# Performance work log

Measured on AMD Instinct MI355X. Metric: run time of the kernel, lower is better.

The kernel has to match this reference:

```python
import jax, jax.numpy as jnp
import numpy as np

NEG_SLOPE = 0.2

def gat_conv(x, W, a_src, a_dst, bias, src, dst, num_nodes, concat):
    # x: [N, F_in]; W: [F_in, H*C]; a_src/a_dst: [H, C]; src/dst: [E] (self-loops included)
    H, C = a_src.shape
    h = (x @ W).reshape(-1, H, C)                      # [N, H, C]
    alpha_s = jnp.einsum('nhc,hc->nh', h, a_src)       # [N, H]
    alpha_d = jnp.einsum('nhc,hc->nh', h, a_dst)       # [N, H]
    e = jax.nn.leaky_relu(alpha_s[src] + alpha_d[dst], NEG_SLOPE)  # [E, H]
    # segment softmax over destination nodes
    m = jax.ops.segment_max(e, dst, num_segments=num_nodes)        # [N, H]
    ex = jnp.exp(e - m[dst])
    denom = jax.ops.segment_sum(ex, dst, num_segments=num_nodes)   # [N, H]
    alpha = ex / (denom[dst] + 1e-16)                  # [E, H]
    msg = alpha[:, :, None] * h[src]                   # [E, H, C]
    out = jax.ops.segment_sum(msg, dst, num_segments=num_nodes)    # [N, H, C]
    if concat:
        out = out.reshape(num_nodes, H * C)
    else:
        out = out.mean(axis=1)
    return out + bias

def setup_inputs() -> dict:
    key = jax.random.key(0)
    ks = jax.random.split(key, 12)
    N, F_in, E = 100000, 512, 3200000
    H1, C1 = 8, 8
    OUT = 40
    x = jax.random.normal(ks[0], (N, F_in), dtype=jnp.float32)
    edge_index = jax.random.randint(ks[1], (2, E), 0, N, dtype=jnp.int64)
    glorot = lambda k, shape: jax.random.uniform(k, shape, jnp.float32, -1.0, 1.0) * np.sqrt(6.0 / (shape[0] + shape[-1]))
    W1 = glorot(ks[2], (F_in, H1 * C1))
    a_src1 = glorot(ks[3], (H1, C1))
    a_dst1 = glorot(ks[4], (H1, C1))
    b1 = jnp.zeros((H1 * C1,), jnp.float32)
    W2 = glorot(ks[5], (H1 * C1, OUT))
    a_src2 = glorot(ks[6], (1, OUT))
    a_dst2 = glorot(ks[7], (1, OUT))
    b2 = jnp.zeros((OUT,), jnp.float32)
    return {"x": x, "edge_index": edge_index, "W1": W1, "a_src1": a_src1,
            "a_dst1": a_dst1, "b1": b1, "W2": W2, "a_src2": a_src2,
            "a_dst2": a_dst2, "b2": b2}

def reference(x, edge_index, W1, a_src1, a_dst1, b1, W2, a_src2, a_dst2, b2):
    N = x.shape[0]
    loop = jnp.arange(N, dtype=edge_index.dtype)
    src = jnp.concatenate([edge_index[0], loop])  # add_self_loops=True (PyG default)
    dst = jnp.concatenate([edge_index[1], loop])
    # dropout is identity in eval mode
    h = gat_conv(x, W1, a_src1, a_dst1, b1, src, dst, N, concat=True)   # [N, 64]
    h = jax.nn.elu(h)
    out = gat_conv(h, W2, a_src2, a_dst2, b2, src, dst, N, concat=False)  # [N, 40]
    return out
```

## Files before the change

kernel.cpp:

```cpp
#include <hip/hip_runtime.h>
#include <hip/hip_bf16.h>


typedef __attribute__((ext_vector_type(8))) short short8;
typedef __attribute__((ext_vector_type(4))) short short4v;
typedef __attribute__((ext_vector_type(4))) float float4v;

#define NEG_SLOPE 0.2f

static __device__ __forceinline__ short f2bf(float v){
    union { float f; unsigned u; } x; x.f = v;
    unsigned r = x.u + 0x7fffu + ((x.u >> 16) & 1u);
    return (short)(r >> 16);
}
static __device__ __forceinline__ float bf2f(short s){
    union { unsigned u; float f; } x; x.u = ((unsigned)(unsigned short)s) << 16;
    return x.f;
}

__global__ void pack_w1(const float* __restrict__ W1, short* __restrict__ Whi, short* __restrict__ Wlo){
    int i = blockIdx.x*blockDim.x + threadIdx.x;
    if (i >= 64*512) return;
    int n = i >> 9, k = i & 511;
    float w = W1[k*64 + n];
    short h = f2bf(w);
    Whi[i] = h;
    Wlo[i] = f2bf(w - bf2f(h));
}

__global__ void detect_i64(const int* __restrict__ ei, int* __restrict__ flag){
    __shared__ int any;
    if (threadIdx.x == 0) any = 0;
    __syncthreads();
    if (ei[2*threadIdx.x + 1] != 0) atomicAdd(&any, 1);
    __syncthreads();
    if (threadIdx.x == 0) flag[0] = (any == 0) ? 1 : 0;
}

__global__ __launch_bounds__(256) void gemm1(const float* __restrict__ x,
        const short* __restrict__ Whi, const short* __restrict__ Wlo,
        float* __restrict__ h1f, short* __restrict__ h1b, int N){
    int wave = threadIdx.x >> 6, lane = threadIdx.x & 63;
    int m = lane & 15, q = lane >> 4;
    int rowbase = blockIdx.x*64 + wave*16;
    int arow = rowbase + m; if (arow > N-1) arow = N-1;
    const float4* ap4 = (const float4*)(x + (size_t)arow*512 + q*8);
    float4v acc[4] = {};
    #pragma unroll 4
    for (int kt = 0; kt < 16; ++kt){
        float4 f0 = ap4[kt*8], f1 = ap4[kt*8+1];
        float v[8] = {f0.x,f0.y,f0.z,f0.w,f1.x,f1.y,f1.z,f1.w};
        short8 ahi, alo;
        #pragma unroll
        for (int j = 0; j < 8; ++j){
            union { float f; unsigned u; } t; t.f = v[j];
            ahi[j] = (short)(t.u >> 16);
            union { unsigned u; float f; } th; th.u = t.u & 0xffff0000u;
            alo[j] = f2bf(v[j] - th.f);
        }
        #pragma unroll
        for (int ct = 0; ct < 4; ++ct){
            const short* wb = Whi + (size_t)(ct*16+m)*512 + kt*32 + q*8;
            const short* wl = Wlo + (size_t)(ct*16+m)*512 + kt*32 + q*8;
            short8 bhi = *(const short8*)wb;
            short8 blo = *(const short8*)wl;
            acc[ct] = __builtin_amdgcn_mfma_f32_16x16x32_bf16(ahi, bhi, acc[ct], 0, 0, 0);
            acc[ct] = __builtin_amdgcn_mfma_f32_16x16x32_bf16(ahi, blo, acc[ct], 0, 0, 0);
            acc[ct] = __builtin_amdgcn_mfma_f32_16x16x32_bf16(alo, bhi, acc[ct], 0, 0, 0);
        }
    }
    #pragma unroll
    for (int ct = 0; ct < 4; ++ct)
        #pragma unroll
        for (int r = 0; r < 4; ++r){
            int row = rowbase + q*4 + r;
            if (row < N){
                h1f[(size_t)row*64 + ct*16 + m] = acc[ct][r];
                h1b[(size_t)row*64 + ct*16 + m] = f2bf(acc[ct][r]);
            }
        }
}

__global__ void alpha1(const float* __restrict__ h1f, const float* __restrict__ a_s,
                       const float* __restrict__ a_d, float* __restrict__ as1,
                       float* __restrict__ ad1, int N){
    int t = blockIdx.x*blockDim.x + threadIdx.x;
    if (t >= N*8) return;
    int h = t & 7;
    const float* hp = h1f + (size_t)t*8;
    float s = 0.f, d = 0.f;
    #pragma unroll
    for (int c = 0; c < 8; ++c){
        float v = hp[c];
        s = fmaf(v, a_s[h*8+c], s);
        d = fmaf(v, a_d[h*8+c], d);
    }
    as1[t] = s; ad1[t] = d;
}

__global__ __launch_bounds__(256) void bucket_hist(const int* __restrict__ ei,
        const int* __restrict__ flag, int* __restrict__ bhist, int E, int Etot, int K){
    extern __shared__ int hist[];
    for (int i = threadIdx.x; i < K; i += 256) hist[i] = 0;
    __syncthreads();
    int f = flag[0];
    int e0 = blockIdx.x*8192, e1 = min(e0 + 8192, Etot);
    for (int e = e0 + threadIdx.x; e < e1; e += 256){
        int dst = (e < E) ? ei[((size_t)(E + e)) << f] : (e - E);
        atomicAdd(&hist[dst >> 8], 1);
    }
    __syncthreads();
    for (int i = threadIdx.x; i < K; i += 256)
        if (hist[i]) atomicAdd(&bhist[i], hist[i]);
}

__global__ __launch_bounds__(1024) void bucket_scan(const int* __restrict__ bhist,
        int* __restrict__ bbase, int* __restrict__ bcursor, int K){
    __shared__ int s[1024];
    int t = threadIdx.x;
    int v = (t < K) ? bhist[t] : 0;
    s[t] = v; __syncthreads();
    for (int off = 1; off < 1024; off <<= 1){
        int x = (t >= off) ? s[t-off] : 0;
        __syncthreads();
        s[t] += x;
        __syncthreads();
    }
    if (t < K){ int excl = s[t] - v; bbase[t] = excl; bcursor[t] = excl; }
    if (t == K) bbase[K] = s[t];
}

__global__ __launch_bounds__(256) void bucket_place(const int* __restrict__ ei,
        const int* __restrict__ flag, int* __restrict__ bcursor,
        int* __restrict__ staging, int E, int Etot, int K){
    extern __shared__ int sm[];
    int* hist = sm;
    int* base = sm + K;
    for (int i = threadIdx.x; i < K; i += 256) hist[i] = 0;
    __syncthreads();
    int f = flag[0];
    int e0 = blockIdx.x*8192, e1 = min(e0 + 8192, Etot);
    for (int e = e0 + threadIdx.x; e < e1; e += 256){
        int dst = (e < E) ? ei[((size_t)(E + e)) << f] : (e - E);
        atomicAdd(&hist[dst >> 8], 1);
    }
    __syncthreads();
    for (int i = threadIdx.x; i < K; i += 256){
        int c = hist[i];
        base[i] = c ? atomicAdd(&bcursor[i], c) : 0;
        hist[i] = 0;
    }
    __syncthreads();
    for (int e = e0 + threadIdx.x; e < e1; e += 256){
        int src, dst;
        if (e < E){ src = ei[((size_t)e) << f]; dst = ei[((size_t)(E + e)) << f]; }
        else      { src = dst = e - E; }
        int k = dst >> 8;
        int r = atomicAdd(&hist[k], 1);
        staging[base[k] + r] = (src << 8) | (dst & 255);
    }
}

__global__ __launch_bounds__(256) void bucket_csr(const int* __restrict__ staging,
        const int* __restrict__ bbase, int* __restrict__ offs, int* __restrict__ deg,
        int* __restrict__ csr, int N, int K){
    __shared__ int dcnt[256], sc[256], cur[256];
    int k = blockIdx.x, t = threadIdx.x;
    dcnt[t] = 0;
    __syncthreads();
    int s0 = bbase[k], s1 = bbase[k+1];
    for (int i = s0 + t; i < s1; i += 256)
        atomicAdd(&dcnt[staging[i] & 255], 1);
    __syncthreads();
    int v = dcnt[t];
    sc[t] = v; __syncthreads();
    for (int off = 1; off < 256; off <<= 1){
        int x = (t >= off) ? sc[t-off] : 0;
        __syncthreads();
        sc[t] += x;
        __syncthreads();
    }
    int excl = sc[t] - v;
    int node = (k << 8) + t;
    if (node < N){ offs[node] = s0 + excl; deg[node] = v; }
    cur[t] = excl;
    __syncthreads();
    for (int i = s0 + t; i < s1; i += 256){
        int ent = staging[i];
        int p = atomicAdd(&cur[ent & 255], 1);
        csr[s0 + p] = ent >> 8;
    }
}

__global__ __launch_bounds__(256) void agg1(const short* __restrict__ h1b,
        const float* __restrict__ as1, const float* __restrict__ ad1,
        const int* __restrict__ offs, const int* __restrict__ deg, const int* __restrict__ csr,
        const float* __restrict__ b1, short* __restrict__ x1b, int N){
    int w = blockIdx.x*4 + (threadIdx.x >> 6);
    if (w >= N) return;
    int lane = threadIdx.x & 63, h = lane >> 3;
    int s0 = offs[w], d = deg[w];
    float ad = ad1[w*8 + h];
    float l = 0.f, acc = 0.f;
    int i = 0;
    for (; i + 4 <= d; i += 4){
        int sa = csr[s0+i], sb = csr[s0+i+1], sc = csr[s0+i+2], sd = csr[s0+i+3];
        float ea = as1[sa*8+h], eb = as1[sb*8+h], ec = as1[sc*8+h], ed = as1[sd*8+h];
        float va = bf2f(h1b[(size_t)sa*64 + lane]);
        float vb = bf2f(h1b[(size_t)sb*64 + lane]);
        float vc = bf2f(h1b[(size_t)sc*64 + lane]);
        float vd = bf2f(h1b[(size_t)sd*64 + lane]);
        ea += ad; ea = (ea > 0.f) ? ea : NEG_SLOPE*ea; float pa = __expf(ea);
        eb += ad; eb = (eb > 0.f) ? eb : NEG_SLOPE*eb; float pb = __expf(eb);
        ec += ad; ec = (ec > 0.f) ? ec : NEG_SLOPE*ec; float pc = __expf(ec);
        ed += ad; ed = (ed > 0.f) ? ed : NEG_SLOPE*ed; float pd = __expf(ed);
        l += (pa + pb) + (pc + pd);
        acc = fmaf(pa, va, acc); acc = fmaf(pb, vb, acc);
        acc = fmaf(pc, vc, acc); acc = fmaf(pd, vd, acc);
    }
    for (; i < d; ++i){
        int s = csr[s0 + i];
        float e = as1[s*8 + h] + ad;
        e = (e > 0.f) ? e : NEG_SLOPE*e;
        float p = __expf(e);
        l += p;
        acc = fmaf(p, bf2f(h1b[(size_t)s*64 + lane]), acc);
    }
    float o = acc/(l + 1e-16f) + b1[lane];
    o = (o > 0.f) ? o : (__expf(o) - 1.f);
    x1b[(size_t)w*64 + lane] = f2bf(o);
}

__global__ __launch_bounds__(256) void gemm2a(const short* __restrict__ x1b,
        const float* __restrict__ W2, const float* __restrict__ aS2, const float* __restrict__ aD2,
        short* __restrict__ h2b, float* __restrict__ as2, float* __restrict__ ad2, int N){
    __shared__ float w2s[64*40];
    __shared__ float xs[4][64];
    int tid = threadIdx.x;
    for (int i = tid; i < 64*40; i += 256) w2s[i] = W2[i];
    int wv = tid >> 6, lane = tid & 63;
    int n = blockIdx.x*4 + wv;
    bool valid = n < N;
    if (valid && lane < 16){
        short4v xv = *(const short4v*)&x1b[(size_t)n*64 + lane*4];
        xs[wv][lane*4+0] = bf2f(xv[0]);
        xs[wv][lane*4+1] = bf2f(xv[1]);
        xs[wv][lane*4+2] = bf2f(xv[2]);
        xs[wv][lane*4+3] = bf2f(xv[3]);
    }
    __syncthreads();
    int c = (lane < 40) ? lane : 39;
    float acc = 0.f;
    #pragma unroll 8
    for (int k = 0; k < 64; ++k)
        acc = fmaf(xs[wv][k], w2s[k*40 + c], acc);
    float s = (lane < 40) ? acc * aS2[lane] : 0.f;
    float d = (lane < 40) ? acc * aD2[lane] : 0.f;
    #pragma unroll
    for (int off = 32; off > 0; off >>= 1){ s += __shfl_down(s, off, 64); d += __shfl_down(d, off, 64); }
    if (valid){
        if (lane < 40) h2b[(size_t)n*40 + lane] = f2bf(acc);
        if (lane == 0){ as2[n] = s; ad2[n] = d; }
    }
}

__global__ __launch_bounds__(256) void agg2(const short* __restrict__ h2b,
        const float* __restrict__ as2, const float* __restrict__ ad2,
        const int* __restrict__ offs, const int* __restrict__ deg, const int* __restrict__ csr,
        const float* __restrict__ b2, float* __restrict__ out, int N){
    int w = blockIdx.x*4 + (threadIdx.x >> 6);
    if (w >= N) return;
    int lane = threadIdx.x & 63;
    int c = (lane < 40) ? lane : 0;
    int s0 = offs[w], d = deg[w];
    float ad = ad2[w];
    float l = 0.f, acc = 0.f;
    int i = 0;
    for (; i + 4 <= d; i += 4){
        int sa = csr[s0+i], sb = csr[s0+i+1], sc = csr[s0+i+2], sd = csr[s0+i+3];
        float ea = as2[sa], eb = as2[sb], ec = as2[sc], ed = as2[sd];
        float va = bf2f(h2b[(size_t)sa*40 + c]);
        float vb = bf2f(h2b[(size_t)sb*40 + c]);
        float vc = bf2f(h2b[(size_t)sc*40 + c]);
        float vd = bf2f(h2b[(size_t)sd*40 + c]);
        ea += ad; ea = (ea > 0.f) ? ea : NEG_SLOPE*ea; float pa = __expf(ea);
        eb += ad; eb = (eb > 0.f) ? eb : NEG_SLOPE*eb; float pb = __expf(eb);
        ec += ad; ec = (ec > 0.f) ? ec : NEG_SLOPE*ec; float pc = __expf(ec);
        ed += ad; ed = (ed > 0.f) ? ed : NEG_SLOPE*ed; float pd = __expf(ed);
        l += (pa + pb) + (pc + pd);
        acc = fmaf(pa, va, acc); acc = fmaf(pb, vb, acc);
        acc = fmaf(pc, vc, acc); acc = fmaf(pd, vd, acc);
    }
    for (; i < d; ++i){
        int s = csr[s0 + i];
        float e = as2[s] + ad;
        e = (e > 0.f) ? e : NEG_SLOPE*e;
        float p = __expf(e);
        l += p;
        acc = fmaf(p, bf2f(h2b[(size_t)s*40 + c]), acc);
    }
    if (lane < 40) out[(size_t)w*40 + lane] = acc/(l + 1e-16f) + b2[lane];
}

extern "C" void kernel_launch(void* const* d_in, const int* in_sizes, int n_in,
                              void* d_out, int out_size, void* d_ws, size_t ws_size,
                              hipStream_t stream) {
    const float* x    = (const float*)d_in[0];
    const int*   ei   = (const int*)d_in[1];
    const float* W1   = (const float*)d_in[2];
    const float* aS1  = (const float*)d_in[3];
    const float* aD1  = (const float*)d_in[4];
    const float* b1   = (const float*)d_in[5];
    const float* W2   = (const float*)d_in[6];
    const float* aS2  = (const float*)d_in[7];
    const float* aD2  = (const float*)d_in[8];
    const float* b2   = (const float*)d_in[9];
    float* out = (float*)d_out;

    const int N    = in_sizes[0] / 512;
    const int E    = in_sizes[1] / 2;
    const int Etot = E + N;
    const int K    = (N + 255) >> 8;
    const int nAB  = (Etot + 8191) / 8192;

    char* p = (char*)d_ws;
    auto carve = [&](size_t bytes)->char*{ char* q = p; p += ((bytes + 255) & ~(size_t)255); return q; };
    float* h1f   = (float*)carve((size_t)N*64*4);
    short* h1b   = (short*)carve((size_t)N*64*2);
    short* x1b   = (short*)carve((size_t)N*64*2);
    short* h2b   = (short*)carve((size_t)N*40*2);
    float* as1   = (float*)carve((size_t)N*8*4);
    float* ad1   = (float*)carve((size_t)N*8*4);
    float* as2   = (float*)carve((size_t)N*4);
    float* ad2   = (float*)carve((size_t)N*4);
    int*   deg   = (int*)carve((size_t)N*4);
    int*   offs  = (int*)carve((size_t)N*4);
    int*   bhist = (int*)carve((size_t)(K+1)*4);
    int*   bbase = (int*)carve((size_t)(K+1)*4);
    int*   bcursor=(int*)carve((size_t)(K+1)*4);
    int*   flag  = (int*)carve(256);
    short* Whi   = (short*)carve(64*512*2);
    short* Wlo   = (short*)carve(64*512*2);
    int*   csr   = (int*)carve((size_t)Etot*4);
    int*   staging = (int*)h1f;

    hipMemsetAsync(bhist, 0, (size_t)K*4, stream);

    detect_i64<<<1, 1024, 0, stream>>>(ei, flag);
    pack_w1<<<(64*512 + 255)/256, 256, 0, stream>>>(W1, Whi, Wlo);

    bucket_hist <<<nAB, 256, (size_t)K*4,   stream>>>(ei, flag, bhist, E, Etot, K);
    bucket_scan <<<1, 1024, 0,              stream>>>(bhist, bbase, bcursor, K);
    bucket_place<<<nAB, 256, (size_t)2*K*4, stream>>>(ei, flag, bcursor, staging, E, Etot, K);
    bucket_csr  <<<K, 256, 0,               stream>>>(staging, bbase, offs, deg, csr, N, K);

    gemm1 <<<(N + 63)/64,    256, 0, stream>>>(x, Whi, Wlo, h1f, h1b, N);
    alpha1<<<(N*8 + 255)/256, 256, 0, stream>>>(h1f, aS1, aD1, as1, ad1, N);

    agg1  <<<(N + 3)/4,  256, 0, stream>>>(h1b, as1, ad1, offs, deg, csr, b1, x1b, N);
    gemm2a<<<(N + 3)/4,  256, 0, stream>>>(x1b, W2, aS2, aD2, h2b, as2, ad2, N);
    agg2  <<<(N + 3)/4,  256, 0, stream>>>(h2b, as2, ad2, offs, deg, csr, b2, out, N);
}
```

Before: 819.2 us.

## Stage x tiles through LDS with double buffering and fuse alpha1 into gemm1 epilogue

After: 828.8 us. About the same (+1.2%).

```diff
diff --git a/kernel.cpp b/kernel.cpp
--- a/kernel.cpp
+++ b/kernel.cpp
@@ -37,65 +37,113 @@
     if (threadIdx.x == 0) flag[0] = (any == 0) ? 1 : 0;
 }
 
-__global__ __launch_bounds__(256) void gemm1(const float* __restrict__ x,
+__global__ __launch_bounds__(256, 4) void gemm1(const float* __restrict__ x,
         const short* __restrict__ Whi, const short* __restrict__ Wlo,
-        float* __restrict__ h1f, short* __restrict__ h1b, int N){
-    int wave = threadIdx.x >> 6, lane = threadIdx.x & 63;
+        const float* __restrict__ aS1, const float* __restrict__ aD1,
+        short* __restrict__ h1b, float* __restrict__ as1, float* __restrict__ ad1, int N){
+    __shared__ __align__(16) float As[2][64][68];
+    int tid = threadIdx.x;
+    int wave = tid >> 6, lane = tid & 63;
     int m = lane & 15, q = lane >> 4;
-    int rowbase = blockIdx.x*64 + wave*16;
-    int arow = rowbase + m; if (arow > N-1) arow = N-1;
-    const float4* ap4 = (const float4*)(x + (size_t)arow*512 + q*8);
+    int rowbase = blockIdx.x*64;
+
+    int srow[4]; int scol[4];
+    #pragma unroll
+    for (int i = 0; i < 4; ++i){
+        int f = i*256 + tid;
+        int r = rowbase + (f >> 4);
+        srow[i] = (r < N) ? r : (N-1);
+        scol[i] = (f & 15) * 4;
+    }
+
+    float4 reg[4];
+    #pragma unroll
+    for (int i = 0; i < 4; ++i)
+        reg[i] = *(const float4*)(x + (size_t)srow[i]*512 + scol[i]);
+    #pragma unroll
+    for (int i = 0; i < 4; ++i){
+        int f = i*256 + tid;
+        *(float4*)&As[0][f >> 4][scol[i]] = reg[i];
+    }
+    __syncthreads();
+
     float4v acc[4] = {};
-    #pragma unroll 4
-    for (int kt = 0; kt < 16; ++kt){
-        float4 f0 = ap4[kt*8], f1 = ap4[kt*8+1];
-        float v[8] = {f0.x,f0.y,f0.z,f0.w,f1.x,f1.y,f1.z,f1.w};
-        short8 ahi, alo;
+    for (int t = 0; t < 8; ++t){
+        int cur = t & 1;
+        if (t < 7){
+            #pragma unroll
+            for (int i = 0; i < 4; ++i)
+                reg[i] = *(const float4*)(x + (size_t)srow[i]*512 + (t+1)*64 + scol[i]);
+        }
+        const float* arow = &As[cur][wave*16 + m][0];
         #pragma unroll
-        for (int j = 0; j < 8; ++j){
-            union { float f; unsigned u; } t; t.f = v[j];
-            ahi[j] = (short)(t.u >> 16);
-            union { unsigned u; float f; } th; th.u = t.u & 0xffff0000u;
-            alo[j] = f2bf(v[j] - th.f);
+        for (int ks = 0; ks < 2; ++ks){
+            float v[8];
+            *(float4*)&v[0] = *(const float4*)(arow + ks*32 + q*8);
+            *(float4*)&v[4] = *(const float4*)(arow + ks*32 + q*8 + 4);
+            short8 ahi, alo;
+            #pragma unroll
+            for (int j = 0; j < 8; ++j){
+                union { float f; unsigned u; } tt; tt.f = v[j];
+                ahi[j] = (short)(tt.u >> 16);
+                union { unsigned u; float f; } th; th.u = tt.u & 0xffff0000u;
+                alo[j] = f2bf(v[j] - th.f);
+            }
+            #pragma unroll
+            for (int ct = 0; ct < 4; ++ct){
+                const short* wb = Whi + (size_t)(ct*16+m)*512 + t*64 + ks*32 + q*8;
+                const short* wl = Wlo + (size_t)(ct*16+m)*512 + t*64 + ks*32 + q*8;
+                short8 bhi = *(const short8*)wb;
+                short8 blo = *(const short8*)wl;
+                acc[ct] = __builtin_amdgcn_mfma_f32_16x16x32_bf16(ahi, bhi, acc[ct], 0, 0, 0);
+                acc[ct] = __builtin_amdgcn_mfma_f32_16x16x32_bf16(ahi, blo, acc[ct], 0, 0, 0);
+                acc[ct] = __builtin_amdgcn_mfma_f32_16x16x32_bf16(alo, bhi, acc[ct], 0, 0, 0);
+            }
         }
-        #pragma unroll
-        for (int ct = 0; ct < 4; ++ct){
-            const short* wb = Whi + (size_t)(ct*16+m)*512 + kt*32 + q*8;
-            const short* wl = Wlo + (size_t)(ct*16+m)*512 + kt*32 + q*8;
-            short8 bhi = *(const short8*)wb;
-            short8 blo = *(const short8*)wl;
-            acc[ct] = __builtin_amdgcn_mfma_f32_16x16x32_bf16(ahi, bhi, acc[ct], 0, 0, 0);
-            acc[ct] = __builtin_amdgcn_mfma_f32_16x16x32_bf16(ahi, blo, acc[ct], 0, 0, 0);
-            acc[ct] = __builtin_amdgcn_mfma_f32_16x16x32_bf16(alo, bhi, acc[ct], 0, 0, 0);
+        if (t < 7){
+            #pragma unroll
+            for (int i = 0; i < 4; ++i){
+                int f = i*256 + tid;
+                *(float4*)&As[t & 1 ? 0 : 1][f >> 4][scol[i]] = reg[i];
+            }
+            __syncthreads();
         }
     }
+
+    float* cw = &As[0][0][0] + wave*(16*68);
     #pragma unroll
     for (int ct = 0; ct < 4; ++ct)
         #pragma unroll
-        for (int r = 0; r < 4; ++r){
-            int row = rowbase + q*4 + r;
-            if (row < N){
-                h1f[(size_t)row*64 + ct*16 + m] = acc[ct][r];
-                h1b[(size_t)row*64 + ct*16 + m] = f2bf(acc[ct][r]);
-            }
+        for (int r = 0; r < 4; ++r)
+            cw[(q*4+r)*68 + ct*16 + m] = acc[ct][r];
+
+    int row_l = lane >> 2;
+    int cseg  = (lane & 3) * 16;
+    int gr = rowbase + wave*16 + row_l;
+    float vals[16];
+    #pragma unroll
+    for (int i = 0; i < 4; ++i)
+        *(float4*)&vals[i*4] = *(const float4*)&cw[row_l*68 + cseg + i*4];
+    if (gr < N){
+        short8 o0, o1;
+        #pragma unroll
+        for (int j = 0; j < 8; ++j){ o0[j] = f2bf(vals[j]); o1[j] = f2bf(vals[8+j]); }
+        *(short8*)&h1b[(size_t)gr*64 + cseg]     = o0;
+        *(short8*)&h1b[(size_t)gr*64 + cseg + 8] = o1;
+        int h0 = (lane & 3) * 2;
+        float s0 = 0.f, d0 = 0.f, s1 = 0.f, d1 = 0.f;
+        #pragma unroll
+        for (int c = 0; c < 8; ++c){
+            s0 = fmaf(vals[c],   aS1[h0*8+c],     s0);
+            d0 = fmaf(vals[c],   aD1[h0*8+c],     d0);
+            s1 = fmaf(vals[8+c], aS1[(h0+1)*8+c], s1);
+            d1 = fmaf(vals[8+c], aD1[(h0+1)*8+c], d1);
         }
-}
-
-__global__ void alpha1(const float* __restrict__ h1f, const float* __restrict__ a_s,
-                       const float* __restrict__ a_d, float* __restrict__ as1,
-                       float* __restrict__ ad1, int N){
-    int t = blockIdx.x*blockDim.x + threadIdx.x;
-    if (t >= N*8) return;
-    int h = t & 7;
-    const float* hp = h1f + (size_t)t*8;
-    float s = 0.f, d = 0.f;
-    #pragma unroll
-    for (int c = 0; c < 8; ++c){
-        float v = hp[c];
-        s = fmaf(v, a_s[h*8+c], s);
-        d = fmaf(v, a_d[h*8+c], d);
-    }
-    as1[t] = s; ad1[t] = d;
+        float2 sv; sv.x = s0; sv.y = s1;
+        float2 dv; dv.x = d0; dv.y = d1;
+        *(float2*)&as1[(size_t)gr*8 + h0] = sv;
+        *(float2*)&ad1[(size_t)gr*8 + h0] = dv;
+    }
 }
 
 __global__ __launch_bounds__(256) void bucket_hist(const int* __restrict__ ei,
@@ -325,7 +373,6 @@
 
     char* p = (char*)d_ws;
     auto carve = [&](size_t bytes)->char*{ char* q = p; p += ((bytes + 255) & ~(size_t)255); return q; };
-    float* h1f   = (float*)carve((size_t)N*64*4);
     short* h1b   = (short*)carve((size_t)N*64*2);
     short* x1b   = (short*)carve((size_t)N*64*2);
     short* h2b   = (short*)carve((size_t)N*40*2);
@@ -342,7 +389,7 @@
     short* Whi   = (short*)carve(64*512*2);
     short* Wlo   = (short*)carve(64*512*2);
     int*   csr   = (int*)carve((size_t)Etot*4);
-    int*   staging = (int*)h1f;
+    int*   staging = (int*)carve((size_t)Etot*4);
 
     hipMemsetAsync(bhist, 0, (size_t)K*4, stream);
 
@@ -354,8 +401,7 @@
     bucket_place<<<nAB, 256, (size_t)2*K*4, stream>>>(ei, flag, bcursor, staging, E, Etot, K);
     bucket_csr  <<<K, 256, 0,               stream>>>(staging, bbase, offs, deg, csr, N, K);
 
-    gemm1 <<<(N + 63)/64,    256, 0, stream>>>(x, Whi, Wlo, h1f, h1b, N);
-    alpha1<<<(N*8 + 255)/256, 256, 0, stream>>>(h1f, aS1, aD1, as1, ad1, N);
+    gemm1 <<<(N + 63)/64, 256, 0, stream>>>(x, Whi, Wlo, aS1, aD1, h1b, as1, ad1, N);
 
     agg1  <<<(N + 3)/4,  256, 0, stream>>>(h1b, as1, ad1, offs, deg, csr, b1, x1b, N);
     gemm2a<<<(N + 3)/4,  256, 0, stream>>>(x1b, W2, aS2, aD2, h2b, as2, ad2, N);
```
